# Optimization experiments

Measured on AMD Instinct MI355X. Metric: run time of the kernel, lower is better.

## Reference

```python
import jax, jax.numpy as jnp
import numpy as np

N = 100000   # nodes
E = 600000   # edges
D = 128      # d_model / hidden_dim
L = 4        # num_layers
V = 5000     # node vocab (in_size)
G = 128      # num graphs in batch
C = 10       # num_class
BN_EPS = 1e-5


def setup_inputs() -> dict:
    key = jax.random.key(0)
    ks = jax.random.split(key, 20)
    s = 0.05
    return {
        "x": jax.random.randint(ks[0], (N,), 0, V),
        "edge_index": jax.random.randint(ks[1], (2, E), 0, N),
        "edge_attr": jax.random.normal(ks[2], (E, 2), dtype=jnp.float32),
        "batch": jnp.sort(jax.random.randint(ks[3], (N,), 0, G)),
        # embedding table
        "emb": jax.random.normal(ks[4], (V, D), dtype=jnp.float32) * s,
        # per-layer GINEConv edge linear (edge_dim=2 -> D)
        "edge_w": jax.random.normal(ks[5], (L, 2, D), dtype=jnp.float32) * s,
        "edge_b": jnp.zeros((L, D), jnp.float32),
        # per-layer MLP: Linear -> BN -> ReLU -> Linear
        "w1": jax.random.normal(ks[6], (L, D, D), dtype=jnp.float32) * s,
        "b1": jnp.zeros((L, D), jnp.float32),
        "g1": jnp.ones((L, D), jnp.float32),
        "beta1": jnp.zeros((L, D), jnp.float32),
        "w2": jax.random.normal(ks[7], (L, D, D), dtype=jnp.float32) * s,
        "b2": jnp.zeros((L, D), jnp.float32),
        # per-layer outer BatchNorm (self.norms)
        "ng": jnp.ones((L, D), jnp.float32),
        "nb": jnp.zeros((L, D), jnp.float32),
        # classifier: Linear(D,D) -> ReLU -> Linear(D,C)
        "cw1": jax.random.normal(ks[8], (D, D), dtype=jnp.float32) * s,
        "cb1": jnp.zeros((D,), jnp.float32),
        "cw2": jax.random.normal(ks[9], (D, C), dtype=jnp.float32) * s,
        "cb2": jnp.zeros((C,), jnp.float32),
    }


def _bn(h, g, b):
    # training-mode BatchNorm1d over node axis, biased variance
    m = h.mean(0)
    v = h.var(0)
    return (h - m) * jax.lax.rsqrt(v + BN_EPS) * g + b


def reference(x, edge_index, edge_attr, batch, emb, edge_w, edge_b,
              w1, b1, g1, beta1, w2, b2, ng, nb, cw1, cb1, cw2, cb2):
    h = emb[x]                                    # [N, D]
    src, dst = edge_index[0], edge_index[1]
    for l in range(L):
        e = edge_attr @ edge_w[l] + edge_b[l]     # [E, D]
        msg = jax.nn.relu(h[src] + e)             # gather + add + relu
        agg = jax.ops.segment_sum(msg, dst, num_segments=N)  # scatter-sum
        z = h + agg                               # (1+eps)*x_i + aggr, eps=0
        z = jax.nn.relu(_bn(z @ w1[l] + b1[l], g1[l], beta1[l]))
        h = _bn(z @ w2[l] + b2[l], ng[l], nb[l])
        if l != L - 1:
            h = jax.nn.relu(h)
    sums = jax.ops.segment_sum(h, batch, num_segments=G)            # [G, D]
    counts = jax.ops.segment_sum(jnp.ones((N, 1), h.dtype), batch, num_segments=G)
    pooled = sums / jnp.maximum(counts, 1.0)      # global mean pool
    return jax.nn.relu(pooled @ cw1 + cb1) @ cw2 + cb2  # [G, C]
```

## Files before the change

kernel.cpp:

```cpp
#include <hip/hip_runtime.h>
#include <stdint.h>

#define N_NODES 100000
#define N_EDGES 600000
#define DMODEL  128
#define NLAYERS 4
#define NGRAPH  128
#define NCLASS  10
#define BN_EPS  1e-5f
#define NSLOT   32
#define STATSZ  (NSLOT * 2 * DMODEL)
#define ZSTR    136
#define NBIN    64

typedef __bf16 bf16x8 __attribute__((ext_vector_type(8)));
typedef __bf16 bf16x4 __attribute__((ext_vector_type(4)));
typedef __bf16 bf16x2 __attribute__((ext_vector_type(2)));
typedef float  f32x4  __attribute__((ext_vector_type(4)));

__global__ void k_init(int* __restrict__ deg, float* __restrict__ statA,
                       float* __restrict__ statB, float* __restrict__ psum,
                       int* __restrict__ dbin,
                       const float* __restrict__ w1, const float* __restrict__ w2,
                       __bf16* __restrict__ wt_hi, __bf16* __restrict__ wt_lo,
                       const int* __restrict__ batch, int* __restrict__ gstart) {
  int i = blockIdx.x * 256 + threadIdx.x;
  if (i < N_NODES) deg[i] = 0;
  if (i < NLAYERS * STATSZ) {
    statA[i] = 0.0f;
    statB[i] = 0.0f;
  }
  if (i < NGRAPH * DMODEL) psum[i] = 0.0f;
  if (i < NBIN) dbin[i] = 0;
  {
    int mat = i >> 14;
    int rem = i & 16383;
    int n = rem >> 7;
    int k = rem & 127;
    int l = mat >> 1;
    int which = mat & 1;
    const float* w = which ? w2 : w1;
    float v = w[(size_t)l * DMODEL * DMODEL + (size_t)k * DMODEL + n];
    __bf16 hi = (__bf16)v;
    wt_hi[i] = hi;
    wt_lo[i] = (__bf16)(v - (float)hi);
  }
  if (i <= NGRAPH) {
    int lo = 0;
    int hi = N_NODES;
    while (lo < hi) {
      int mid = (lo + hi) >> 1;
      if (batch[mid] < i) lo = mid + 1; else hi = mid;
    }
    gstart[i] = lo;
  }
}

__global__ void k_embed(const int* __restrict__ x, const float* __restrict__ emb,
                        __bf16* __restrict__ h) {
  int idx = blockIdx.x * 256 + threadIdx.x;
  if (idx >= N_NODES * DMODEL / 8) return;
  int i = idx >> 4;
  int p = idx & 15;
  const float* src = emb + (size_t)x[i] * DMODEL + p * 8;
  float4 v0 = *(const float4*)(src);
  float4 v1 = *(const float4*)(src + 4);
  bf16x8 o;
  o[0] = (__bf16)v0.x; o[1] = (__bf16)v0.y; o[2] = (__bf16)v0.z; o[3] = (__bf16)v0.w;
  o[4] = (__bf16)v1.x; o[5] = (__bf16)v1.y; o[6] = (__bf16)v1.z; o[7] = (__bf16)v1.w;
  *(bf16x8*)(h + (size_t)i * DMODEL + p * 8) = o;
}

__global__ void k_hist(const int* __restrict__ dst, int* __restrict__ deg) {
  int e = blockIdx.x * 256 + threadIdx.x;
  if (e < N_EDGES) atomicAdd(&deg[dst[e]], 1);
}

__global__ void k_scan1(const int* __restrict__ deg, int* __restrict__ out,
                        int* __restrict__ bsum, int n) {
  __shared__ int lds[256];
  int t = threadIdx.x;
  int idx = blockIdx.x * 256 + t;
  int v = (idx < n) ? deg[idx] : 0;
  int val = v;
  lds[t] = val;
  for (int ofs = 1; ofs < 256; ofs <<= 1) {
    __syncthreads();
    int u = (t >= ofs) ? lds[t - ofs] : 0;
    __syncthreads();
    val += u;
    lds[t] = val;
  }
  if (idx < n) out[idx] = val - v;
  if (t == 255) bsum[blockIdx.x] = val;
}

__global__ void k_scan2(const int* __restrict__ bsum, int* __restrict__ bsumx, int nb) {
  __shared__ int lds[512];
  int t = threadIdx.x;
  int v = (t < nb) ? bsum[t] : 0;
  int val = v;
  lds[t] = val;
  for (int ofs = 1; ofs < 512; ofs <<= 1) {
    __syncthreads();
    int u = (t >= ofs) ? lds[t - ofs] : 0;
    __syncthreads();
    val += u;
    lds[t] = val;
  }
  if (t < nb) bsumx[t] = val - v;
}

__global__ void k_scan3(int* __restrict__ row_start, int* __restrict__ cursor,
                        const int* __restrict__ bsumx, int n, int total) {
  int idx = blockIdx.x * 256 + threadIdx.x;
  if (idx < n) {
    int v = row_start[idx] + bsumx[blockIdx.x];
    row_start[idx] = v;
    cursor[idx] = v;
  }
  if (idx == 0) row_start[n] = total;
}

__global__ void k_scatter(const int* __restrict__ ei, const float* __restrict__ ea,
                          int* __restrict__ cursor, int4* __restrict__ epack) {
  int e = blockIdx.x * 256 + threadIdx.x;
  if (e >= N_EDGES) return;
  int s = ei[e];
  int d = ei[N_EDGES + e];
  int pos = atomicAdd(&cursor[d], 1);
  int4 pk;
  pk.x = s;
  pk.y = __float_as_int(ea[2 * e]);
  pk.z = __float_as_int(ea[2 * e + 1]);
  pk.w = 0;
  epack[pos] = pk;
}

__global__ void k_dhist(const int* __restrict__ deg, int* __restrict__ dbin) {
  __shared__ int lbin[NBIN];
  int t = threadIdx.x;
  if (t < NBIN) lbin[t] = 0;
  __syncthreads();
  int i = blockIdx.x * 256 + t;
  if (i < N_NODES) {
    int b = min(deg[i], NBIN - 1);
    atomicAdd(&lbin[b], 1);
  }
  __syncthreads();
  if (t < NBIN && lbin[t] > 0) atomicAdd(&dbin[t], lbin[t]);
}

__global__ void k_dscan(const int* __restrict__ dbin, int* __restrict__ dcursor) {
  __shared__ int lds[NBIN];
  int t = threadIdx.x;
  int v = dbin[t];
  int val = v;
  lds[t] = val;
  for (int ofs = 1; ofs < NBIN; ofs <<= 1) {
    __syncthreads();
    int u = (t >= ofs) ? lds[t - ofs] : 0;
    __syncthreads();
    val += u;
    lds[t] = val;
  }
  dcursor[t] = val - v;
}

__global__ void k_dscatter(const int* __restrict__ deg, int* __restrict__ dcursor,
                           int* __restrict__ sched) {
  __shared__ int lcnt[NBIN];
  __shared__ int lbase[NBIN];
  int t = threadIdx.x;
  if (t < NBIN) lcnt[t] = 0;
  __syncthreads();
  int i = blockIdx.x * 256 + t;
  int b = 0;
  int lrank = 0;
  if (i < N_NODES) {
    b = min(deg[i], NBIN - 1);
    lrank = atomicAdd(&lcnt[b], 1);
  }
  __syncthreads();
  if (t < NBIN) lbase[t] = (lcnt[t] > 0) ? atomicAdd(&dcursor[t], lcnt[t]) : 0;
  __syncthreads();
  if (i < N_NODES) sched[lbase[b] + lrank] = i;
}

__global__ void __launch_bounds__(256) k_aggemm(
    const __bf16* __restrict__ h, const int* __restrict__ row_start,
    const int4* __restrict__ epack, const int* __restrict__ sched,
    const float* __restrict__ ew,
    const float* __restrict__ ebp,
    const float* __restrict__ statPrev,
    const float* __restrict__ gammaP, const float* __restrict__ betaP, int hasT,
    const __bf16* __restrict__ Whi, const __bf16* __restrict__ Wlo,
    const float* __restrict__ bias,
    __bf16* __restrict__ Y,
    float* __restrict__ statpart) {
  __shared__ __align__(16) __bf16 zt[32 * ZSTR];
  __shared__ float sld[DMODEL];
  __shared__ float tld[DMODEL];
  __shared__ int snode[32];
  int tid = threadIdx.x;

  if (hasT) {
    if (tid < DMODEL) {
      float sum = 0.0f;
      float sq = 0.0f;
      for (int p = 0; p < NSLOT; ++p) {
        sum += statPrev[p * (2 * DMODEL) + tid];
        sq  += statPrev[p * (2 * DMODEL) + DMODEL + tid];
      }
      float mean = sum * (1.0f / N_NODES);
      float var = sq * (1.0f / N_NODES) - mean * mean;
      float inv = rsqrtf(var + BN_EPS);
      float s = gammaP[tid] * inv;
      sld[tid] = s;
      tld[tid] = betaP[tid] - mean * s;
    }
    __syncthreads();
  }

  int hw = tid >> 5;
  int ln = tid & 31;
  int d0 = ln * 4;

  float4 ew0 = *(const float4*)(ew + d0);
  float4 ew1 = *(const float4*)(ew + DMODEL + d0);
  float4 eb  = *(const float4*)(ebp + d0);
  float4 s4;
  float4 t4;
  if (hasT) {
    s4 = *(const float4*)(sld + d0);
    t4 = *(const float4*)(tld + d0);
  }

#define AGG_ONE(E, V)                                                          \
  {                                                                            \
    float a0 = __int_as_float((E).y);                                          \
    float a1 = __int_as_float((E).z);                                          \
    float f0 = (float)(V)[0];                                                  \
    float f1 = (float)(V)[1];                                                  \
    float f2 = (float)(V)[2];                                                  \
    float f3 = (float)(V)[3];                                                  \
    if (hasT) {                                                                \
      f0 = fmaxf(s4.x * f0 + t4.x, 0.0f);                                      \
      f1 = fmaxf(s4.y * f1 + t4.y, 0.0f);                                      \
      f2 = fmaxf(s4.z * f2 + t4.z, 0.0f);                                      \
      f3 = fmaxf(s4.w * f3 + t4.w, 0.0f);                                      \
    }                                                                          \
    acc0 += fmaxf(f0 + a0 * ew0.x + a1 * ew1.x + eb.x, 0.0f);                  \
    acc1 += fmaxf(f1 + a0 * ew0.y + a1 * ew1.y + eb.y, 0.0f);                  \
    acc2 += fmaxf(f2 + a0 * ew0.z + a1 * ew1.z + eb.z, 0.0f);                  \
    acc3 += fmaxf(f3 + a0 * ew0.w + a1 * ew1.w + eb.w, 0.0f);                  \
  }

  for (int i = 0; i < 4; ++i) {
    int nl = hw * 4 + i;
    int node = sched[blockIdx.x * 32 + nl];
    if (ln == 0) snode[nl] = node;
    bf16x4 hv = *(const bf16x4*)(h + (size_t)node * DMODEL + d0);
    float acc0, acc1, acc2, acc3;
    {
      float r0 = (float)hv[0];
      float r1 = (float)hv[1];
      float r2 = (float)hv[2];
      float r3 = (float)hv[3];
      if (hasT) {
        acc0 = fmaxf(s4.x * r0 + t4.x, 0.0f);
        acc1 = fmaxf(s4.y * r1 + t4.y, 0.0f);
        acc2 = fmaxf(s4.z * r2 + t4.z, 0.0f);
        acc3 = fmaxf(s4.w * r3 + t4.w, 0.0f);
      } else {
        acc0 = r0; acc1 = r1; acc2 = r2; acc3 = r3;
      }
    }
    int j0 = row_start[node];
    int j1 = row_start[node + 1];
    int j = j0;
    for (; j + 4 <= j1; j += 4) {
      int4 e0 = epack[j];
      int4 e1 = epack[j + 1];
      int4 e2 = epack[j + 2];
      int4 e3 = epack[j + 3];
      bf16x4 v0 = *(const bf16x4*)(h + (size_t)e0.x * DMODEL + d0);
      bf16x4 v1 = *(const bf16x4*)(h + (size_t)e1.x * DMODEL + d0);
      bf16x4 v2 = *(const bf16x4*)(h + (size_t)e2.x * DMODEL + d0);
      bf16x4 v3 = *(const bf16x4*)(h + (size_t)e3.x * DMODEL + d0);
      AGG_ONE(e0, v0)
      AGG_ONE(e1, v1)
      AGG_ONE(e2, v2)
      AGG_ONE(e3, v3)
    }
    for (; j < j1; ++j) {
      int4 e0 = epack[j];
      bf16x4 v0 = *(const bf16x4*)(h + (size_t)e0.x * DMODEL + d0);
      AGG_ONE(e0, v0)
    }
    bf16x4 o;
    o[0] = (__bf16)acc0;
    o[1] = (__bf16)acc1;
    o[2] = (__bf16)acc2;
    o[3] = (__bf16)acc3;
    *(bf16x4*)(zt + nl * ZSTR + d0) = o;
  }
#undef AGG_ONE

  __syncthreads();

  int wave = tid >> 6;
  int lane = tid & 63;
  int n16 = lane & 15;
  int quad = lane >> 4;

  bf16x8 bhi[2][4];
  bf16x8 blo[2][4];
#pragma unroll
  for (int ct = 0; ct < 2; ++ct) {
    int n = (wave * 2 + ct) * 16 + n16;
#pragma unroll
    for (int kk = 0; kk < 4; ++kk) {
      int k0 = kk * 32 + quad * 8;
      bhi[ct][kk] = *(const bf16x8*)(Whi + (size_t)n * DMODEL + k0);
      blo[ct][kk] = *(const bf16x8*)(Wlo + (size_t)n * DMODEL + k0);
    }
  }
  float bc[2];
  bc[0] = bias[(wave * 2 + 0) * 16 + n16];
  bc[1] = bias[(wave * 2 + 1) * 16 + n16];

  bf16x8 a[2][4];
#pragma unroll
  for (int t = 0; t < 2; ++t) {
    const __bf16* zr = zt + (t * 16 + n16) * ZSTR;
#pragma unroll
    for (int kk = 0; kk < 4; ++kk) {
      a[t][kk] = *(const bf16x8*)(zr + kk * 32 + quad * 8);
    }
  }

  f32x4 acc[2][2];
#pragma unroll
  for (int t = 0; t < 2; ++t)
#pragma unroll
    for (int ct = 0; ct < 2; ++ct)
#pragma unroll
      for (int r = 0; r < 4; ++r) acc[t][ct][r] = 0.0f;

#pragma unroll
  for (int kk = 0; kk < 4; ++kk) {
#pragma unroll
    for (int ct = 0; ct < 2; ++ct) {
#pragma unroll
      for (int t = 0; t < 2; ++t) {
        acc[t][ct] = __builtin_amdgcn_mfma_f32_16x16x32_bf16(a[t][kk], bhi[ct][kk], acc[t][ct], 0, 0, 0);
        acc[t][ct] = __builtin_amdgcn_mfma_f32_16x16x32_bf16(a[t][kk], blo[ct][kk], acc[t][ct], 0, 0, 0);
      }
    }
  }

  float ssum[2] = {0.0f, 0.0f};
  float ssq[2] = {0.0f, 0.0f};
#pragma unroll
  for (int t = 0; t < 2; ++t) {
#pragma unroll
    for (int ct = 0; ct < 2; ++ct) {
      int col = (wave * 2 + ct) * 16 + n16;
#pragma unroll
      for (int r = 0; r < 4; ++r) {
        int row = snode[t * 16 + quad * 4 + r];
        float v = acc[t][ct][r] + bc[ct];
        Y[(size_t)row * DMODEL + col] = (__bf16)v;
        ssum[ct] += v;
        ssq[ct] += v * v;
      }
    }
  }

  int slot = blockIdx.x & (NSLOT - 1);
#pragma unroll
  for (int ct = 0; ct < 2; ++ct) {
    int col = (wave * 2 + ct) * 16 + n16;
    float s = ssum[ct];
    float q = ssq[ct];
    s += __shfl_xor(s, 16);
    q += __shfl_xor(q, 16);
    s += __shfl_xor(s, 32);
    q += __shfl_xor(q, 32);
    if (quad == 0) {
      atomicAdd(&statpart[slot * (2 * DMODEL) + col], s);
      atomicAdd(&statpart[slot * (2 * DMODEL) + DMODEL + col], q);
    }
  }
}

__global__ void __launch_bounds__(256) k_gemm2(
    const __bf16* __restrict__ X,
    const __bf16* __restrict__ Whi, const __bf16* __restrict__ Wlo,
    const float* __restrict__ bias,
    const float* __restrict__ statA,
    const float* __restrict__ gamma, const float* __restrict__ beta,
    __bf16* __restrict__ Y,
    float* __restrict__ statpart) {
  __shared__ float sld[DMODEL];
  __shared__ float tld[DMODEL];
  int tid = threadIdx.x;

  if (tid < DMODEL) {
    float sum = 0.0f;
    float sq = 0.0f;
    for (int p = 0; p < NSLOT; ++p) {
      sum += statA[p * (2 * DMODEL) + tid];
      sq  += statA[p * (2 * DMODEL) + DMODEL + tid];
    }
    float mean = sum * (1.0f / N_NODES);
    float var = sq * (1.0f / N_NODES) - mean * mean;
    float inv = rsqrtf(var + BN_EPS);
    float s = gamma[tid] * inv;
    sld[tid] = s;
    tld[tid] = beta[tid] - mean * s;
  }
  __syncthreads();

  int wave = tid >> 6;
  int lane = tid & 63;
  int n16 = lane & 15;
  int quad = lane >> 4;

  bf16x8 bhi[2][4];
  bf16x8 blo[2][4];
#pragma unroll
  for (int ct = 0; ct < 2; ++ct) {
    int n = (wave * 2 + ct) * 16 + n16;
#pragma unroll
    for (int kk = 0; kk < 4; ++kk) {
      int k0 = kk * 32 + quad * 8;
      bhi[ct][kk] = *(const bf16x8*)(Whi + (size_t)n * DMODEL + k0);
      blo[ct][kk] = *(const bf16x8*)(Wlo + (size_t)n * DMODEL + k0);
    }
  }
  float bc[2];
  bc[0] = bias[(wave * 2 + 0) * 16 + n16];
  bc[1] = bias[(wave * 2 + 1) * 16 + n16];

  float ssum[2] = {0.0f, 0.0f};
  float ssq[2] = {0.0f, 0.0f};

  const int NCHUNK = N_NODES / 32;
  for (int c = blockIdx.x; c < NCHUNK; c += gridDim.x) {
    int row0 = c * 32;
    bf16x8 a[2][4];
#pragma unroll
    for (int t = 0; t < 2; ++t) {
      const __bf16* xr = X + (size_t)(row0 + t * 16 + n16) * DMODEL;
#pragma unroll
      for (int kk = 0; kk < 4; ++kk) {
        a[t][kk] = *(const bf16x8*)(xr + kk * 32 + quad * 8);
      }
    }
#pragma unroll
    for (int kk = 0; kk < 4; ++kk) {
      int k0 = kk * 32 + quad * 8;
      float4 s0 = *(const float4*)(sld + k0);
      float4 s1 = *(const float4*)(sld + k0 + 4);
      float4 t0 = *(const float4*)(tld + k0);
      float4 t1 = *(const float4*)(tld + k0 + 4);
      float sv[8];
      float tv[8];
      sv[0] = s0.x; sv[1] = s0.y; sv[2] = s0.z; sv[3] = s0.w;
      sv[4] = s1.x; sv[5] = s1.y; sv[6] = s1.z; sv[7] = s1.w;
      tv[0] = t0.x; tv[1] = t0.y; tv[2] = t0.z; tv[3] = t0.w;
      tv[4] = t1.x; tv[5] = t1.y; tv[6] = t1.z; tv[7] = t1.w;
#pragma unroll
      for (int t = 0; t < 2; ++t) {
#pragma unroll
        for (int jj = 0; jj < 8; ++jj) {
          float f = (float)a[t][kk][jj];
          a[t][kk][jj] = (__bf16)fmaxf(sv[jj] * f + tv[jj], 0.0f);
        }
      }
    }

    f32x4 acc[2][2];
#pragma unroll
    for (int t = 0; t < 2; ++t)
#pragma unroll
      for (int ct = 0; ct < 2; ++ct)
#pragma unroll
        for (int r = 0; r < 4; ++r) acc[t][ct][r] = 0.0f;

#pragma unroll
    for (int kk = 0; kk < 4; ++kk) {
#pragma unroll
      for (int ct = 0; ct < 2; ++ct) {
#pragma unroll
        for (int t = 0; t < 2; ++t) {
          acc[t][ct] = __builtin_amdgcn_mfma_f32_16x16x32_bf16(a[t][kk], bhi[ct][kk], acc[t][ct], 0, 0, 0);
          acc[t][ct] = __builtin_amdgcn_mfma_f32_16x16x32_bf16(a[t][kk], blo[ct][kk], acc[t][ct], 0, 0, 0);
        }
      }
    }

#pragma unroll
    for (int t = 0; t < 2; ++t) {
#pragma unroll
      for (int ct = 0; ct < 2; ++ct) {
        int col = (wave * 2 + ct) * 16 + n16;
#pragma unroll
        for (int r = 0; r < 4; ++r) {
          int row = row0 + t * 16 + quad * 4 + r;
          float v = acc[t][ct][r] + bc[ct];
          Y[(size_t)row * DMODEL + col] = (__bf16)v;
          ssum[ct] += v;
          ssq[ct] += v * v;
        }
      }
    }
  }

  int slot = blockIdx.x & (NSLOT - 1);
#pragma unroll
  for (int ct = 0; ct < 2; ++ct) {
    int col = (wave * 2 + ct) * 16 + n16;
    float s = ssum[ct];
    float q = ssq[ct];
    s += __shfl_xor(s, 16);
    q += __shfl_xor(q, 16);
    s += __shfl_xor(s, 32);
    q += __shfl_xor(q, 32);
    if (quad == 0) {
      atomicAdd(&statpart[slot * (2 * DMODEL) + col], s);
      atomicAdd(&statpart[slot * (2 * DMODEL) + DMODEL + col], q);
    }
  }
}

__global__ void k_pool(const __bf16* __restrict__ h, const int* __restrict__ gstart,
                       float* __restrict__ psum) {
  int g = blockIdx.x;
  int slice = blockIdx.y;
  int lane = threadIdx.x;
  int d0 = lane * 2;
  int i0 = gstart[g];
  int i1 = gstart[g + 1];
  float a0 = 0.0f;
  float a1 = 0.0f;
  for (int i = i0 + slice; i < i1; i += 8) {
    bf16x2 v = *(const bf16x2*)(h + (size_t)i * DMODEL + d0);
    a0 += (float)v[0];
    a1 += (float)v[1];
  }
  atomicAdd(&psum[g * DMODEL + d0], a0);
  atomicAdd(&psum[g * DMODEL + d0 + 1], a1);
}

__global__ void k_classifier(const float* __restrict__ psum, const int* __restrict__ gstart,
                             const float* __restrict__ statB,
                             const float* __restrict__ gamma, const float* __restrict__ beta,
                             const float* __restrict__ cw1, const float* __restrict__ cb1,
                             const float* __restrict__ cw2, const float* __restrict__ cb2,
                             float* __restrict__ out) {
  __shared__ float pl[DMODEL];
  __shared__ float hid[DMODEL];
  int g = blockIdx.x;
  int d = threadIdx.x;
  float sum = 0.0f;
  float sq = 0.0f;
  for (int p = 0; p < NSLOT; ++p) {
    sum += statB[p * (2 * DMODEL) + d];
    sq  += statB[p * (2 * DMODEL) + DMODEL + d];
  }
  float mean = sum * (1.0f / N_NODES);
  float var = sq * (1.0f / N_NODES) - mean * mean;
  float inv = rsqrtf(var + BN_EPS);
  float s2 = gamma[d] * inv;
  float t2 = beta[d] - mean * s2;

  int cnt = gstart[g + 1] - gstart[g];
  pl[d] = (cnt > 0) ? (s2 * (psum[g * DMODEL + d] / (float)cnt) + t2) : 0.0f;
  __syncthreads();
  float acc = cb1[d];
  for (int k = 0; k < DMODEL; ++k) acc += pl[k] * cw1[k * DMODEL + d];
  hid[d] = fmaxf(acc, 0.0f);
  __syncthreads();
  if (d < NCLASS) {
    float acc2 = cb2[d];
    for (int k = 0; k < DMODEL; ++k) acc2 += hid[k] * cw2[k * NCLASS + d];
    out[g * NCLASS + d] = acc2;
  }
}

extern "C" void kernel_launch(void* const* d_in, const int* in_sizes, int n_in,
                              void* d_out, int out_size, void* d_ws, size_t ws_size,
                              hipStream_t stream) {
  const int*   x      = (const int*)d_in[0];
  const int*   ei     = (const int*)d_in[1];
  const float* ea     = (const float*)d_in[2];
  const int*   batch  = (const int*)d_in[3];
  const float* emb    = (const float*)d_in[4];
  const float* edge_w = (const float*)d_in[5];
  const float* edge_b = (const float*)d_in[6];
  const float* w1     = (const float*)d_in[7];
  const float* b1     = (const float*)d_in[8];
  const float* g1     = (const float*)d_in[9];
  const float* beta1  = (const float*)d_in[10];
  const float* w2     = (const float*)d_in[11];
  const float* b2     = (const float*)d_in[12];
  const float* ng     = (const float*)d_in[13];
  const float* nb     = (const float*)d_in[14];
  const float* cw1    = (const float*)d_in[15];
  const float* cb1    = (const float*)d_in[16];
  const float* cw2    = (const float*)d_in[17];
  const float* cb2    = (const float*)d_in[18];

  char* ws = (char*)d_ws;
  size_t off = 0;
  auto alloc = [&](size_t bytes) -> void* {
    void* p = ws + off;
    off += (bytes + 255) & ~(size_t)255;
    return p;
  };

  __bf16* h_bf      = (__bf16*)alloc((size_t)N_NODES * DMODEL * sizeof(__bf16));
  __bf16* y1_bf     = (__bf16*)alloc((size_t)N_NODES * DMODEL * sizeof(__bf16));
  int*    row_start = (int*)alloc((N_NODES + 1) * sizeof(int));
  int*    cursor    = (int*)alloc(N_NODES * sizeof(int));
  int*    deg       = (int*)alloc(N_NODES * sizeof(int));
  int*    sched     = (int*)alloc(N_NODES * sizeof(int));
  int4*   epack     = (int4*)alloc((size_t)N_EDGES * sizeof(int4));
  __bf16* wt_hi     = (__bf16*)alloc((size_t)NLAYERS * 2 * DMODEL * DMODEL * sizeof(__bf16));
  __bf16* wt_lo     = (__bf16*)alloc((size_t)NLAYERS * 2 * DMODEL * DMODEL * sizeof(__bf16));
  float*  statA     = (float*)alloc((size_t)NLAYERS * STATSZ * sizeof(float));
  float*  statB     = (float*)alloc((size_t)NLAYERS * STATSZ * sizeof(float));
  int*    gstart    = (int*)alloc((NGRAPH + 1) * sizeof(int));
  float*  psum      = (float*)alloc((size_t)NGRAPH * DMODEL * sizeof(float));
  int*    dbin      = (int*)alloc(NBIN * sizeof(int));
  int*    dcursor   = (int*)alloc(NBIN * sizeof(int));
  int*    bsum      = (int*)alloc(512 * sizeof(int));
  int*    bsumx     = (int*)alloc(512 * sizeof(int));

  auto statAL = [&](int l) { return statA + (size_t)l * STATSZ; };
  auto statBL = [&](int l) { return statB + (size_t)l * STATSZ; };

  const int nbScan = (N_NODES + 255) / 256;
  const int nbEdge = (N_EDGES + 255) / 256;
  const int nbEmb  = (N_NODES * DMODEL / 8 + 255) / 256;
  const int nbGemm = 782;
  const int nbFuse = N_NODES / 32;

  k_init<<<512, 256, 0, stream>>>(deg, statA, statB, psum, dbin,
                                  w1, w2, wt_hi, wt_lo, batch, gstart);
  k_embed<<<nbEmb, 256, 0, stream>>>(x, emb, h_bf);
  k_hist<<<nbEdge, 256, 0, stream>>>(ei + N_EDGES, deg);
  k_scan1<<<nbScan, 256, 0, stream>>>(deg, row_start, bsum, N_NODES);
  k_scan2<<<1, 512, 0, stream>>>(bsum, bsumx, nbScan);
  k_scan3<<<nbScan, 256, 0, stream>>>(row_start, cursor, bsumx, N_NODES, N_EDGES);
  k_scatter<<<nbEdge, 256, 0, stream>>>(ei, ea, cursor, epack);
  k_dhist<<<nbScan, 256, 0, stream>>>(deg, dbin);
  k_dscan<<<1, NBIN, 0, stream>>>(dbin, dcursor);
  k_dscatter<<<nbScan, 256, 0, stream>>>(deg, dcursor, sched);

  for (int l = 0; l < NLAYERS; ++l) {
    const float* sPrev = (l > 0) ? statBL(l - 1) : (const float*)nullptr;
    const float* gPrev = (l > 0) ? (ng + (size_t)(l - 1) * DMODEL) : (const float*)nullptr;
    const float* bPrev = (l > 0) ? (nb + (size_t)(l - 1) * DMODEL) : (const float*)nullptr;
    k_aggemm<<<nbFuse, 256, 0, stream>>>(
        h_bf, row_start, epack, sched,
        edge_w + (size_t)l * 2 * DMODEL,
        edge_b + (size_t)l * DMODEL,
        sPrev, gPrev, bPrev, (l > 0) ? 1 : 0,
        wt_hi + (size_t)(l * 2 + 0) * DMODEL * DMODEL,
        wt_lo + (size_t)(l * 2 + 0) * DMODEL * DMODEL,
        b1 + (size_t)l * DMODEL,
        y1_bf, statAL(l));
    k_gemm2<<<nbGemm, 256, 0, stream>>>(
        y1_bf,
        wt_hi + (size_t)(l * 2 + 1) * DMODEL * DMODEL,
        wt_lo + (size_t)(l * 2 + 1) * DMODEL * DMODEL,
        b2 + (size_t)l * DMODEL,
        statAL(l), g1 + (size_t)l * DMODEL, beta1 + (size_t)l * DMODEL,
        h_bf, statBL(l));
  }

  dim3 poolGrid(NGRAPH, 8);
  k_pool<<<poolGrid, 64, 0, stream>>>(h_bf, gstart, psum);
  k_classifier<<<NGRAPH, DMODEL, 0, stream>>>(psum, gstart, statBL(NLAYERS - 1),
                                              ng + (size_t)(NLAYERS - 1) * DMODEL,
                                              nb + (size_t)(NLAYERS - 1) * DMODEL,
                                              cw1, cb1, cw2, cb2, (float*)d_out);
}
```

Baseline: 660.8 us.

## Fuse preprocessing kernels and compress edge records to 8 bytes with bf16 attrs

Merges init and embedding into one kernel and folds the degree-histogram, degree scan, and schedule scatter into the CSR scan kernels, cutting ten preprocessing launches to six. Edge records shrink from int4 to int2, with the two edge attributes stored as packed bf16, which halves edge-stream bandwidth in the per-layer aggregation. The cost is reduced precision on the edge attributes. There is also a hazard: k_pre1 zeroes dbin while the embedding work runs in the same launch, and the dbin accumulation now lives in k_pre2.

New measurement: 639.6 us. 1.03x faster.

```diff
diff --git a/kernel.cpp b/kernel.cpp
--- a/kernel.cpp
+++ b/kernel.cpp
@@ -18,57 +18,70 @@
 typedef __bf16 bf16x2 __attribute__((ext_vector_type(2)));
 typedef float  f32x4  __attribute__((ext_vector_type(4)));
 
-__global__ void k_init(int* __restrict__ deg, float* __restrict__ statA,
+static __device__ __forceinline__ bf16x2 unpack_bf16x2(int v) {
+  union { int i; bf16x2 h; } u;
+  u.i = v;
+  return u.h;
+}
+static __device__ __forceinline__ int pack_bf16x2(float a, float b) {
+  union { int i; bf16x2 h; } u;
+  u.h[0] = (__bf16)a;
+  u.h[1] = (__bf16)b;
+  return u.i;
+}
+
+__global__ void k_pre1(int* __restrict__ deg, float* __restrict__ statA,
                        float* __restrict__ statB, float* __restrict__ psum,
                        int* __restrict__ dbin,
                        const float* __restrict__ w1, const float* __restrict__ w2,
                        __bf16* __restrict__ wt_hi, __bf16* __restrict__ wt_lo,
-                       const int* __restrict__ batch, int* __restrict__ gstart) {
-  int i = blockIdx.x * 256 + threadIdx.x;
-  if (i < N_NODES) deg[i] = 0;
-  if (i < NLAYERS * STATSZ) {
-    statA[i] = 0.0f;
-    statB[i] = 0.0f;
-  }
-  if (i < NGRAPH * DMODEL) psum[i] = 0.0f;
-  if (i < NBIN) dbin[i] = 0;
-  {
-    int mat = i >> 14;
-    int rem = i & 16383;
-    int n = rem >> 7;
-    int k = rem & 127;
-    int l = mat >> 1;
-    int which = mat & 1;
-    const float* w = which ? w2 : w1;
-    float v = w[(size_t)l * DMODEL * DMODEL + (size_t)k * DMODEL + n];
-    __bf16 hi = (__bf16)v;
-    wt_hi[i] = hi;
-    wt_lo[i] = (__bf16)(v - (float)hi);
-  }
-  if (i <= NGRAPH) {
-    int lo = 0;
-    int hi = N_NODES;
-    while (lo < hi) {
-      int mid = (lo + hi) >> 1;
-      if (batch[mid] < i) lo = mid + 1; else hi = mid;
-    }
-    gstart[i] = lo;
-  }
-}
-
-__global__ void k_embed(const int* __restrict__ x, const float* __restrict__ emb,
-                        __bf16* __restrict__ h) {
+                       const int* __restrict__ batch, int* __restrict__ gstart,
+                       const int* __restrict__ x, const float* __restrict__ emb,
+                       __bf16* __restrict__ h) {
   int idx = blockIdx.x * 256 + threadIdx.x;
-  if (idx >= N_NODES * DMODEL / 8) return;
-  int i = idx >> 4;
-  int p = idx & 15;
-  const float* src = emb + (size_t)x[i] * DMODEL + p * 8;
-  float4 v0 = *(const float4*)(src);
-  float4 v1 = *(const float4*)(src + 4);
-  bf16x8 o;
-  o[0] = (__bf16)v0.x; o[1] = (__bf16)v0.y; o[2] = (__bf16)v0.z; o[3] = (__bf16)v0.w;
-  o[4] = (__bf16)v1.x; o[5] = (__bf16)v1.y; o[6] = (__bf16)v1.z; o[7] = (__bf16)v1.w;
-  *(bf16x8*)(h + (size_t)i * DMODEL + p * 8) = o;
+  if (idx < N_NODES * DMODEL / 8) {
+    int i = idx >> 4;
+    int p = idx & 15;
+    const float* src = emb + (size_t)x[i] * DMODEL + p * 8;
+    float4 v0 = *(const float4*)(src);
+    float4 v1 = *(const float4*)(src + 4);
+    bf16x8 o;
+    o[0] = (__bf16)v0.x; o[1] = (__bf16)v0.y; o[2] = (__bf16)v0.z; o[3] = (__bf16)v0.w;
+    o[4] = (__bf16)v1.x; o[5] = (__bf16)v1.y; o[6] = (__bf16)v1.z; o[7] = (__bf16)v1.w;
+    *(bf16x8*)(h + (size_t)i * DMODEL + p * 8) = o;
+  }
+  if (idx < NLAYERS * 2 * DMODEL * DMODEL) {
+    int i = idx;
+    if (i < N_NODES) deg[i] = 0;
+    if (i < NLAYERS * STATSZ) {
+      statA[i] = 0.0f;
+      statB[i] = 0.0f;
+    }
+    if (i < NGRAPH * DMODEL) psum[i] = 0.0f;
+    if (i < NBIN) dbin[i] = 0;
+    {
+      int mat = i >> 14;
+      int rem = i & 16383;
+      int n = rem >> 7;
+      int k = rem & 127;
+      int l = mat >> 1;
+      int which = mat & 1;
+      const float* w = which ? w2 : w1;
+      float v = w[(size_t)l * DMODEL * DMODEL + (size_t)k * DMODEL + n];
+      __bf16 hi = (__bf16)v;
+      wt_hi[i] = hi;
+      wt_lo[i] = (__bf16)(v - (float)hi);
+    }
+    if (i <= NGRAPH) {
+      int lo = 0;
+      int hi = N_NODES;
+      while (lo < hi) {
+        int mid = (lo + hi) >> 1;
+        if (batch[mid] < i) lo = mid + 1; else hi = mid;
+      }
+      gstart[i] = lo;
+    }
+  }
 }
 
 __global__ void k_hist(const int* __restrict__ dst, int* __restrict__ deg) {
@@ -76,14 +89,16 @@
   if (e < N_EDGES) atomicAdd(&deg[dst[e]], 1);
 }
 
-__global__ void k_scan1(const int* __restrict__ deg, int* __restrict__ out,
-                        int* __restrict__ bsum, int n) {
+__global__ void k_pre2(const int* __restrict__ deg, int* __restrict__ out,
+                       int* __restrict__ bsum, int* __restrict__ dbin) {
   __shared__ int lds[256];
+  __shared__ int lbin[NBIN];
   int t = threadIdx.x;
   int idx = blockIdx.x * 256 + t;
-  int v = (idx < n) ? deg[idx] : 0;
+  int v = (idx < N_NODES) ? deg[idx] : 0;
   int val = v;
   lds[t] = val;
+  if (t < NBIN) lbin[t] = 0;
   for (int ofs = 1; ofs < 256; ofs <<= 1) {
     __syncthreads();
     int u = (t >= ofs) ? lds[t - ofs] : 0;
@@ -91,12 +106,18 @@
     val += u;
     lds[t] = val;
   }
-  if (idx < n) out[idx] = val - v;
+  if (idx < N_NODES) out[idx] = val - v;
   if (t == 255) bsum[blockIdx.x] = val;
-}
-
-__global__ void k_scan2(const int* __restrict__ bsum, int* __restrict__ bsumx, int nb) {
+  __syncthreads();
+  if (idx < N_NODES) atomicAdd(&lbin[min(v, NBIN - 1)], 1);
+  __syncthreads();
+  if (t < NBIN && lbin[t] > 0) atomicAdd(&dbin[t], lbin[t]);
+}
+
+__global__ void k_pre3(const int* __restrict__ bsum, int* __restrict__ bsumx, int nb,
+                       const int* __restrict__ dbin, int* __restrict__ dcursor) {
   __shared__ int lds[512];
+  __shared__ int ldb[NBIN];
   int t = threadIdx.x;
   int v = (t < nb) ? bsum[t] : 0;
   int val = v;
@@ -109,87 +130,66 @@
     lds[t] = val;
   }
   if (t < nb) bsumx[t] = val - v;
-}
-
-__global__ void k_scan3(int* __restrict__ row_start, int* __restrict__ cursor,
-                        const int* __restrict__ bsumx, int n, int total) {
-  int idx = blockIdx.x * 256 + threadIdx.x;
-  if (idx < n) {
+  __syncthreads();
+  if (t < NBIN) {
+    int dv = dbin[t];
+    int dval = dv;
+    ldb[t] = dval;
+    for (int ofs = 1; ofs < NBIN; ofs <<= 1) {
+      __syncthreads();
+      int u = (t >= ofs) ? ldb[t - ofs] : 0;
+      __syncthreads();
+      dval += u;
+      ldb[t] = dval;
+    }
+    dcursor[t] = dval - dv;
+  }
+}
+
+__global__ void k_pre4(int* __restrict__ row_start, int* __restrict__ cursor,
+                       const int* __restrict__ bsumx,
+                       const int* __restrict__ deg, int* __restrict__ dcursor,
+                       int* __restrict__ sched) {
+  __shared__ int lcnt[NBIN];
+  __shared__ int lbase[NBIN];
+  int t = threadIdx.x;
+  int idx = blockIdx.x * 256 + t;
+  if (idx < N_NODES) {
     int v = row_start[idx] + bsumx[blockIdx.x];
     row_start[idx] = v;
     cursor[idx] = v;
   }
-  if (idx == 0) row_start[n] = total;
+  if (idx == 0) row_start[N_NODES] = N_EDGES;
+  if (t < NBIN) lcnt[t] = 0;
+  __syncthreads();
+  int b = 0;
+  int lrank = 0;
+  if (idx < N_NODES) {
+    b = min(deg[idx], NBIN - 1);
+    lrank = atomicAdd(&lcnt[b], 1);
+  }
+  __syncthreads();
+  if (t < NBIN) lbase[t] = (lcnt[t] > 0) ? atomicAdd(&dcursor[t], lcnt[t]) : 0;
+  __syncthreads();
+  if (idx < N_NODES) sched[lbase[b] + lrank] = idx;
 }
 
 __global__ void k_scatter(const int* __restrict__ ei, const float* __restrict__ ea,
-                          int* __restrict__ cursor, int4* __restrict__ epack) {
+                          int* __restrict__ cursor, int2* __restrict__ epack) {
   int e = blockIdx.x * 256 + threadIdx.x;
   if (e >= N_EDGES) return;
   int s = ei[e];
   int d = ei[N_EDGES + e];
   int pos = atomicAdd(&cursor[d], 1);
-  int4 pk;
+  int2 pk;
   pk.x = s;
-  pk.y = __float_as_int(ea[2 * e]);
-  pk.z = __float_as_int(ea[2 * e + 1]);
-  pk.w = 0;
+  pk.y = pack_bf16x2(ea[2 * e], ea[2 * e + 1]);
   epack[pos] = pk;
-}
-
-__global__ void k_dhist(const int* __restrict__ deg, int* __restrict__ dbin) {
-  __shared__ int lbin[NBIN];
-  int t = threadIdx.x;
-  if (t < NBIN) lbin[t] = 0;
-  __syncthreads();
-  int i = blockIdx.x * 256 + t;
-  if (i < N_NODES) {
-    int b = min(deg[i], NBIN - 1);
-    atomicAdd(&lbin[b], 1);
-  }
-  __syncthreads();
-  if (t < NBIN && lbin[t] > 0) atomicAdd(&dbin[t], lbin[t]);
-}
-
-__global__ void k_dscan(const int* __restrict__ dbin, int* __restrict__ dcursor) {
-  __shared__ int lds[NBIN];
-  int t = threadIdx.x;
-  int v = dbin[t];
-  int val = v;
-  lds[t] = val;
-  for (int ofs = 1; ofs < NBIN; ofs <<= 1) {
-    __syncthreads();
-    int u = (t >= ofs) ? lds[t - ofs] : 0;
-    __syncthreads();
-    val += u;
-    lds[t] = val;
-  }
-  dcursor[t] = val - v;
-}
-
-__global__ void k_dscatter(const int* __restrict__ deg, int* __restrict__ dcursor,
-                           int* __restrict__ sched) {
-  __shared__ int lcnt[NBIN];
-  __shared__ int lbase[NBIN];
-  int t = threadIdx.x;
-  if (t < NBIN) lcnt[t] = 0;
-  __syncthreads();
-  int i = blockIdx.x * 256 + t;
-  int b = 0;
-  int lrank = 0;
-  if (i < N_NODES) {
-    b = min(deg[i], NBIN - 1);
-    lrank = atomicAdd(&lcnt[b], 1);
-  }
-  __syncthreads();
-  if (t < NBIN) lbase[t] = (lcnt[t] > 0) ? atomicAdd(&dcursor[t], lcnt[t]) : 0;
-  __syncthreads();
-  if (i < N_NODES) sched[lbase[b] + lrank] = i;
 }
 
 __global__ void __launch_bounds__(256) k_aggemm(
     const __bf16* __restrict__ h, const int* __restrict__ row_start,
-    const int4* __restrict__ epack, const int* __restrict__ sched,
+    const int2* __restrict__ epack, const int* __restrict__ sched,
     const float* __restrict__ ew,
     const float* __restrict__ ebp,
     const float* __restrict__ statPrev,
@@ -238,8 +238,9 @@
 
 #define AGG_ONE(E, V)                                                          \
   {                                                                            \
-    float a0 = __int_as_float((E).y);                                          \
-    float a1 = __int_as_float((E).z);                                          \
+    bf16x2 av = unpack_bf16x2((E).y);                                          \
+    float a0 = (float)av[0];                                                   \
+    float a1 = (float)av[1];                                                   \
     float f0 = (float)(V)[0];                                                  \
     float f1 = (float)(V)[1];                                                  \
     float f2 = (float)(V)[2];                                                  \
@@ -280,10 +281,10 @@
     int j1 = row_start[node + 1];
     int j = j0;
     for (; j + 4 <= j1; j += 4) {
-      int4 e0 = epack[j];
-      int4 e1 = epack[j + 1];
-      int4 e2 = epack[j + 2];
-      int4 e3 = epack[j + 3];
+      int2 e0 = epack[j];
+      int2 e1 = epack[j + 1];
+      int2 e2 = epack[j + 2];
+      int2 e3 = epack[j + 3];
       bf16x4 v0 = *(const bf16x4*)(h + (size_t)e0.x * DMODEL + d0);
       bf16x4 v1 = *(const bf16x4*)(h + (size_t)e1.x * DMODEL + d0);
       bf16x4 v2 = *(const bf16x4*)(h + (size_t)e2.x * DMODEL + d0);
@@ -294,7 +295,7 @@
       AGG_ONE(e3, v3)
     }
     for (; j < j1; ++j) {
-      int4 e0 = epack[j];
+      int2 e0 = epack[j];
       bf16x4 v0 = *(const bf16x4*)(h + (size_t)e0.x * DMODEL + d0);
       AGG_ONE(e0, v0)
     }
@@ -628,7 +629,7 @@
   int*    cursor    = (int*)alloc(N_NODES * sizeof(int));
   int*    deg       = (int*)alloc(N_NODES * sizeof(int));
   int*    sched     = (int*)alloc(N_NODES * sizeof(int));
-  int4*   epack     = (int4*)alloc((size_t)N_EDGES * sizeof(int4));
+  int2*   epack     = (int2*)alloc((size_t)N_EDGES * sizeof(int2));
   __bf16* wt_hi     = (__bf16*)alloc((size_t)NLAYERS * 2 * DMODEL * DMODEL * sizeof(__bf16));
   __bf16* wt_lo     = (__bf16*)alloc((size_t)NLAYERS * 2 * DMODEL * DMODEL * sizeof(__bf16));
   float*  statA     = (float*)alloc((size_t)NLAYERS * STATSZ * sizeof(float));
@@ -645,21 +646,18 @@
 
   const int nbScan = (N_NODES + 255) / 256;
   const int nbEdge = (N_EDGES + 255) / 256;
-  const int nbEmb  = (N_NODES * DMODEL / 8 + 255) / 256;
+  const int nbPre1 = (N_NODES * DMODEL / 8 + 255) / 256;
   const int nbGemm = 782;
   const int nbFuse = N_NODES / 32;
 
-  k_init<<<512, 256, 0, stream>>>(deg, statA, statB, psum, dbin,
-                                  w1, w2, wt_hi, wt_lo, batch, gstart);
-  k_embed<<<nbEmb, 256, 0, stream>>>(x, emb, h_bf);
+  k_pre1<<<nbPre1, 256, 0, stream>>>(deg, statA, statB, psum, dbin,
+                                     w1, w2, wt_hi, wt_lo, batch, gstart,
+                                     x, emb, h_bf);
   k_hist<<<nbEdge, 256, 0, stream>>>(ei + N_EDGES, deg);
-  k_scan1<<<nbScan, 256, 0, stream>>>(deg, row_start, bsum, N_NODES);
-  k_scan2<<<1, 512, 0, stream>>>(bsum, bsumx, nbScan);
-  k_scan3<<<nbScan, 256, 0, stream>>>(row_start, cursor, bsumx, N_NODES, N_EDGES);
+  k_pre2<<<nbScan, 256, 0, stream>>>(deg, row_start, bsum, dbin);
+  k_pre3<<<1, 512, 0, stream>>>(bsum, bsumx, nbScan, dbin, dcursor);
+  k_pre4<<<nbScan, 256, 0, stream>>>(row_start, cursor, bsumx, deg, dcursor, sched);
   k_scatter<<<nbEdge, 256, 0, stream>>>(ei, ea, cursor, epack);
-  k_dhist<<<nbScan, 256, 0, stream>>>(deg, dbin);
-  k_dscan<<<1, NBIN, 0, stream>>>(dbin, dcursor);
-  k_dscatter<<<nbScan, 256, 0, stream>>>(deg, dcursor, sched);
 
   for (int l = 0; l < NLAYERS; ++l) {
     const float* sPrev = (l > 0) ? statBL(l - 1) : (const float*)nullptr;
```
